# Optimization experiments

Measured on AMD Instinct MI355X. Metric: run time of the kernel, lower is better.

## Reference

```python
import jax, jax.numpy as jnp
import numpy as np

E, H, NGRAM, TM, B, NB = 1024, 16, 2, 512, 4, 32


def setup_inputs() -> dict:
    key = jax.random.key(0)
    ks = jax.random.split(key, 12)
    T3 = (NGRAM + 1) * TM
    s = 0.02
    d = {}
    d["hidden_states"] = jax.random.normal(ks[0], (T3, B, E), jnp.float32)
    d["self_attn_mask"] = jax.random.normal(ks[1], (TM, TM), jnp.float32)
    d["ngram_mask_matrix"] = jax.random.normal(ks[2], (NGRAM, 1, TM, 2 * TM), jnp.float32)
    d["i_buckets_main_stream"] = jax.random.randint(ks[3], (B, TM, TM), 0, NB, jnp.int32)
    d["i_bucket_relative_stream"] = jax.random.randint(ks[4], (B, TM, 2 * TM), 0, NB, jnp.int32)
    d["Wq"] = jax.random.normal(ks[5], (E, E), jnp.float32) * s
    d["bq"] = jnp.zeros((E,), jnp.float32)
    d["Wk"] = jax.random.normal(ks[6], (E, E), jnp.float32) * s
    d["bk"] = jnp.zeros((E,), jnp.float32)
    d["Wv"] = jax.random.normal(ks[7], (E, E), jnp.float32) * s
    d["bv"] = jnp.zeros((E,), jnp.float32)
    d["Wo"] = jax.random.normal(ks[8], (E, E), jnp.float32) * s
    d["bo"] = jnp.zeros((E,), jnp.float32)
    d["Wr"] = jax.random.normal(ks[9], (NB * H, E), jnp.float32) * s
    d["br"] = jnp.zeros((NB * H,), jnp.float32)
    return d


def _lin(x, W, b):
    return x @ W.T + b


def reference(hidden_states, self_attn_mask, ngram_mask_matrix,
              i_buckets_main_stream, i_bucket_relative_stream,
              Wq, bq, Wk, bk, Wv, bv, Wo, bo, Wr, br):
    T3, Bb, Ee = hidden_states.shape
    hd = Ee // H
    Tm = T3 // (NGRAM + 1)
    BH = Bb * H

    # projections; q is pre-scaled as in the torch module
    q = _lin(hidden_states, Wq, bq) * (hd ** -0.5)
    k = _lin(hidden_states, Wk, bk)
    v = _lin(hidden_states, Wv, bv)
    # (T3, B, E) -> (BH, T3, hd)
    q = q.reshape(T3, BH, hd).transpose(1, 0, 2)
    k = k.reshape(T3, BH, hd).transpose(1, 0, 2)
    v = v.reshape(T3, BH, hd).transpose(1, 0, 2)

    q_parts = jnp.split(q, NGRAM + 1, axis=1)
    k_parts = jnp.split(k, NGRAM + 1, axis=1)
    v_parts = jnp.split(v, NGRAM + 1, axis=1)
    h_parts = jnp.split(hidden_states, NGRAM + 1, axis=0)
    q_main, k_main, v_main, h_main = q_parts[0], k_parts[0], v_parts[0], h_parts[0]

    # ---------- main stream ----------
    aw_main = jnp.einsum('btd,bsd->bts', q_main, k_main)  # (BH, Tm, Tm)

    # relative-position logits: per-query learned bucket logits, gathered by bucket id
    vals = _lin(h_main.transpose(1, 0, 2), Wr, br)          # (B, Tm, NB*H)
    vals = vals.reshape(Bb, Tm, NB, H).transpose(0, 3, 1, 2).reshape(BH, Tm, NB)
    idx = jnp.broadcast_to(i_buckets_main_stream[:, None], (Bb, H, Tm, Tm)).reshape(BH, Tm, Tm)
    aw_main = aw_main + jnp.take_along_axis(vals, idx, axis=2) + self_attn_mask

    probs_main = jax.nn.softmax(aw_main.astype(jnp.float32), axis=-1).astype(aw_main.dtype)
    attn_main = jnp.einsum('bts,bsd->btd', probs_main, v_main)   # (BH, Tm, hd)
    attn_main = attn_main.transpose(1, 0, 2).reshape(Tm, Bb, Ee)
    attn_main = _lin(attn_main, Wo, bo)                           # (Tm, B, E)

    # ---------- ngram streams ----------
    q_ng = jnp.stack(q_parts[1:], 0)                              # (N, BH, Tm, hd)
    k_ng = jnp.stack([jnp.concatenate([k_main, kp], axis=1) for kp in k_parts[1:]], 0)  # (N, BH, 2Tm, hd)
    v_ng = jnp.stack([jnp.concatenate([v_main, vp], axis=1) for vp in v_parts[1:]], 0)
    h_ng = jnp.stack(h_parts[1:], 0)                              # (N, Tm, B, E)

    aw_ng = jnp.einsum('nbtc,nbsc->nbts', q_ng, k_ng)             # (N, BH, Tm, 2Tm)

    vals_ng = _lin(h_ng.transpose(0, 2, 1, 3), Wr, br)            # (N, B, Tm, NB*H)
    vals_ng = vals_ng.reshape(NGRAM, Bb, Tm, NB, H).transpose(0, 1, 4, 2, 3).reshape(NGRAM, BH, Tm, NB)
    idx_ng = jnp.broadcast_to(i_bucket_relative_stream[None, :, None],
                              (NGRAM, Bb, H, Tm, 2 * Tm)).reshape(NGRAM, BH, Tm, 2 * Tm)
    aw_ng = aw_ng + jnp.take_along_axis(vals_ng, idx_ng, axis=-1) + ngram_mask_matrix

    probs_ng = jax.nn.softmax(aw_ng.astype(jnp.float32), axis=-1).astype(aw_ng.dtype)
    attn_ng = jnp.einsum('nbts,nbsc->nbtc', probs_ng, v_ng)       # (N, BH, Tm, hd)
    attn_ng = attn_ng.transpose(0, 2, 1, 3).reshape(NGRAM, Tm, Bb, Ee)
    attn_ng = _lin(attn_ng, Wo, bo)                                # (N, Tm, B, E)

    attn = jnp.concatenate([attn_main[None], attn_ng], axis=0).reshape(T3, Bb, Ee)
    return attn
```

## Files before the change

kernel.cpp:

```cpp
#include <hip/hip_runtime.h>
#include <hip/hip_fp16.h>
#include <cstdint>

#define T3   1536
#define TMQ  512
#define BB   4
#define EE   1024
#define HH   16
#define HD   64
#define NBK  32
#define BHH  64

#define LOG2E 1.44269504f
#define SM_SHIFT 4.0f

typedef _Float16 half8 __attribute__((ext_vector_type(8)));
typedef float    f32x4 __attribute__((ext_vector_type(4)));

#define SWZ(r, o) ((o) ^ (((r) & 7) << 4))

__device__ inline void gl_lds16(const void* g, void* l) {
    __builtin_amdgcn_global_load_lds(
        (const __attribute__((address_space(1))) uint32_t*)g,
        (__attribute__((address_space(3))) uint32_t*)l, 16, 0, 0);
}

__global__ __launch_bounds__(256) void cvt_all(
    const float* __restrict__ hs, const float* __restrict__ Wq,
    const float* __restrict__ Wk, const float* __restrict__ Wv,
    const float* __restrict__ Wo, const float* __restrict__ Wr,
    __half* __restrict__ dst)
{
    const long i = (long)blockIdx.x * 256 + threadIdx.x;
    const float* src; long off;
    if (i < 1572864L) { src = hs; off = i; }
    else {
        const long j = i - 1572864L;
        const int  w = (int)(j >> 18);
        const long r = j & 262143L;
        src = (w == 0) ? Wq : (w == 1) ? Wk : (w == 2) ? Wv : (w == 3) ? Wo : Wr;
        off = r;
    }
    const float4 v = ((const float4*)src)[off];
    const __half2 h0 = __floats2half2_rn(v.x, v.y);
    const __half2 h1 = __floats2half2_rn(v.z, v.w);
    uint2 u;
    u.x = *(const unsigned int*)&h0;
    u.y = *(const unsigned int*)&h1;
    ((uint2*)dst)[i] = u;
}

template<int MODE>
__global__ __launch_bounds__(256) void gemm16(
    const __half* __restrict__ A,
    const __half* __restrict__ Wa, const __half* __restrict__ Wb,
    const __half* __restrict__ Wc, const __half* __restrict__ Wd,
    const float* __restrict__ ba, const float* __restrict__ bb,
    const float* __restrict__ bc, const float* __restrict__ bd,
    void* __restrict__ oa, void* __restrict__ ob,
    void* __restrict__ oc, void* __restrict__ od)
{
    __shared__ __half As[128 * 32];
    __shared__ __half Bs[128 * 32];

    const int tid  = threadIdx.x;
    const int w    = tid >> 6, lane = tid & 63;
    const int m0   = blockIdx.y * 128;

    const __half* Wsel; const float* bsel; void* osel;
    float scale, offs; int n0; int sel = 0;
    if (MODE == 0) {
        const int bx = blockIdx.x;
        sel  = (bx < 24) ? (bx >> 3) : 3;
        n0   = (bx < 24) ? (bx & 7) * 128 : (bx - 24) * 128;
        Wsel = sel == 0 ? Wa : (sel == 1 ? Wb : (sel == 2 ? Wc : Wd));
        bsel = sel == 0 ? ba : (sel == 1 ? bb : (sel == 2 ? bc : bd));
        osel = sel == 0 ? oa : (sel == 1 ? ob : (sel == 2 ? oc : od));
        scale = (sel == 0) ? 0.125f * LOG2E : (sel == 3 ? LOG2E : 1.0f);
        offs  = (sel == 3) ? -SM_SHIFT * LOG2E : 0.0f;
    } else {
        n0 = blockIdx.x * 128; Wsel = Wa; bsel = ba; osel = oa;
        scale = 1.0f; offs = 0.0f;
    }

    f32x4 acc[4][4];
    #pragma unroll
    for (int i = 0; i < 4; ++i)
        #pragma unroll
        for (int j = 0; j < 4; ++j) acc[i][j] = (f32x4){0.f, 0.f, 0.f, 0.f};

    const int wr = w >> 1, wc = w & 1;
    const int lrow = lane & 15, lkg = lane >> 4;
    const int a_off0 = (wr * 64 + lrow) * 64 + lkg * 16;
    const int b_off0 = (wc * 64 + lrow) * 64 + lkg * 16;

    const int chunkbase = w * 2048;
    const char* Ab  = (const char*)A;
    const char* Wb8 = (const char*)Wsel;

    for (int k0 = 0; k0 < EE; k0 += 32) {
        #pragma unroll
        for (int i = 0; i < 2; ++i) {
            const int off  = chunkbase + i * 1024 + lane * 16;
            const int row  = off >> 6;
            const int colb = off & 63;
            gl_lds16(Ab  + (size_t)(m0 + row) * 2048 + k0 * 2 + colb,
                     (char*)As + chunkbase + i * 1024);
            gl_lds16(Wb8 + (size_t)(n0 + row) * 2048 + k0 * 2 + colb,
                     (char*)Bs + chunkbase + i * 1024);
        }
        __syncthreads();

        half8 af[4], bf[4];
        #pragma unroll
        for (int m = 0; m < 4; ++m) af[m] = *(const half8*)((const char*)As + a_off0 + m * 1024);
        #pragma unroll
        for (int n = 0; n < 4; ++n) bf[n] = *(const half8*)((const char*)Bs + b_off0 + n * 1024);
        #pragma unroll
        for (int m = 0; m < 4; ++m)
            #pragma unroll
            for (int n = 0; n < 4; ++n)
                acc[m][n] = __builtin_amdgcn_mfma_f32_16x16x32_f16(af[m], bf[n], acc[m][n], 0, 0, 0);
        __syncthreads();
    }

    const int col_l  = lane & 15;
    const int row_l4 = (lane >> 4) * 4;
    #pragma unroll
    for (int n = 0; n < 4; ++n) {
        const int gcol = n0 + wc * 64 + n * 16 + col_l;
        const float bias = bsel[gcol];
        #pragma unroll
        for (int m = 0; m < 4; ++m) {
            #pragma unroll
            for (int j = 0; j < 4; ++j) {
                const int grow = m0 + wr * 64 + m * 16 + row_l4 + j;
                const float cval = (acc[m][n][j] + bias) * scale + offs;
                if (MODE == 0) {
                    const int t3 = grow >> 2, bb2 = grow & 3;
                    if (sel == 3) {
                        const int st = t3 >> 9, tm = t3 & 511;
                        const int nb = gcol >> 4, hh2 = gcol & 15;
                        ((float*)osel)[(((size_t)(st * BHH + bb2 * HH + hh2)) * TMQ + tm) * NBK + nb] = cval;
                    } else {
                        const int hh2 = gcol >> 6, d = gcol & 63;
                        __half* oh = (__half*)osel;
                        const __half hv = __float2half(cval);
                        if (sel == 2)
                            oh[((size_t)((bb2 * HH + hh2) * HD + d)) * T3 + t3] = hv;
                        else
                            oh[(((size_t)(bb2 * HH + hh2)) * T3 + t3) * HD + d] = hv;
                    }
                } else {
                    ((float*)osel)[(size_t)grow * EE + gcol] = cval;
                }
            }
        }
    }
}

__global__ __launch_bounds__(256) void attn_mfma(
    const __half* __restrict__ q, const __half* __restrict__ k,
    const __half* __restrict__ vt, const float* __restrict__ vals,
    const float* __restrict__ self_mask, const float* __restrict__ ngram_mask,
    const int* __restrict__ ibm, const int* __restrict__ ibr,
    __half* __restrict__ attn_pre)
{
    __shared__ __half QP [64 * 64];
    __shared__ __half Ks [64 * 64];
    __shared__ __half Vts[64 * 64];
    __shared__ float  vals_s[64 * NBK];

    const int bid = blockIdx.x;
    const int xcd = bid & 7, rr = bid >> 3;
    int s, bh, qt;
    if (rr < 128) { const int g = xcd * 128 + rr; s = 1 + (g >> 9); bh = (g >> 3) & 63; qt = g & 7; }
    else          { const int mi = xcd * 64 + (rr - 128); s = 0; bh = mi >> 3; qt = mi & 7; }
    const int b = bh >> 4, h = bh & 15;
    const int tid = threadIdx.x;
    const int w = tid >> 6, lane = tid & 63;
    const int lc = lane & 15, lg = lane >> 4;
    const int nch = (s == 0) ? 8 : 16;

    {
        const char* qg = (const char*)(q + ((size_t)bh * T3 + s * TMQ + qt * 64) * HD);
        const char* vg = (const char*)(vals + (((size_t)s * BHH + bh) * TMQ + qt * 64) * NBK);
        #pragma unroll
        for (int p = 0; p < 2; ++p) {
            const int u = tid + p * 256;
            const int row = u >> 3, sub = (u & 7) * 16;
            *(uint4*)((char*)QP + row * 128 + SWZ(row, sub)) = *(const uint4*)(qg + (size_t)u * 16);
            *(uint4*)((char*)vals_s + (size_t)u * 16)        = *(const uint4*)(vg + (size_t)u * 16);
        }
    }

    uint4 ku0, ku1, vu0, vu1;
    int   ix[4][4];
    float mk[4][4];
    {
        const char* kg = (const char*)(k + (size_t)bh * T3 * HD);
        const char* vg = (const char*)(vt + (size_t)bh * HD * T3);
        ku0 = *(const uint4*)(kg + (size_t)tid * 16);
        ku1 = *(const uint4*)(kg + (size_t)(tid + 256) * 16);
        vu0 = *(const uint4*)(vg + (size_t)(tid >> 3) * (T3 * 2) + (tid & 7) * 16);
        vu1 = *(const uint4*)(vg + (size_t)((tid + 256) >> 3) * (T3 * 2) + (tid & 7) * 16);
        #pragma unroll
        for (int j = 0; j < 4; ++j) {
            const int t = qt * 64 + w * 16 + lg * 4 + j;
            const int* ip; const float* mp;
            if (s == 0) { ip = ibm + ((size_t)b * TMQ + t) * TMQ + lc;
                          mp = self_mask + (size_t)t * TMQ + lc; }
            else        { ip = ibr + ((size_t)b * TMQ + t) * (2 * TMQ) + lc;
                          mp = ngram_mask + ((size_t)(s - 1) * TMQ + t) * (2 * TMQ) + lc; }
            #pragma unroll
            for (int n = 0; n < 4; ++n) { ix[j][n] = ip[n * 16]; mk[j][n] = mp[n * 16]; }
        }
    }
    __syncthreads();

    half8 aq[2];
    {
        const int qr = w * 16 + lc;
        const char* qb = (const char*)QP + qr * 128;
        aq[0] = *(const half8*)(qb + SWZ(qr, lg * 16));
        aq[1] = *(const half8*)(qb + SWZ(qr, 64 + lg * 16));
    }

    f32x4 o[4];
    #pragma unroll
    for (int nd = 0; nd < 4; ++nd) o[nd] = (f32x4){0.f, 0.f, 0.f, 0.f};
    float l_p[4] = {0.f, 0.f, 0.f, 0.f};

    for (int c = 0; c < nch; ++c) {
        if (c > 0) __syncthreads();
        {
            const int u0 = tid, u1 = tid + 256;
            const int r0 = u0 >> 3, s0 = (u0 & 7) * 16;
            const int r1 = u1 >> 3, s1 = (u1 & 7) * 16;
            *(uint4*)((char*)Ks  + r0 * 128 + SWZ(r0, s0)) = ku0;
            *(uint4*)((char*)Ks  + r1 * 128 + SWZ(r1, s1)) = ku1;
            *(uint4*)((char*)Vts + r0 * 128 + SWZ(r0, s0)) = vu0;
            *(uint4*)((char*)Vts + r1 * 128 + SWZ(r1, s1)) = vu1;
        }
        __syncthreads();

        if (c + 1 < nch) {
            const int jn  = (c + 1) * 64;
            const int t3n = (jn < TMQ) ? jn : s * TMQ + (jn - TMQ);
            const char* kg = (const char*)(k + ((size_t)bh * T3 + t3n) * HD);
            const char* vg = (const char*)(vt + (size_t)bh * HD * T3 + t3n);
            ku0 = *(const uint4*)(kg + (size_t)tid * 16);
            ku1 = *(const uint4*)(kg + (size_t)(tid + 256) * 16);
            vu0 = *(const uint4*)(vg + (size_t)(tid >> 3) * (T3 * 2) + (tid & 7) * 16);
            vu1 = *(const uint4*)(vg + (size_t)((tid + 256) >> 3) * (T3 * 2) + (tid & 7) * 16);
        }

        f32x4 sc[4];
        #pragma unroll
        for (int n = 0; n < 4; ++n) sc[n] = (f32x4){0.f, 0.f, 0.f, 0.f};
        __builtin_amdgcn_s_setprio(1);
        #pragma unroll
        for (int ks = 0; ks < 2; ++ks) {
            #pragma unroll
            for (int n = 0; n < 4; ++n) {
                const int kr = n * 16 + lc;
                const half8 bk = *(const half8*)((const char*)Ks + kr * 128 + SWZ(kr, ks * 64 + lg * 16));
                sc[n] = __builtin_amdgcn_mfma_f32_16x16x32_f16(aq[ks], bk, sc[n], 0, 0, 0);
            }
        }
        __builtin_amdgcn_s_setprio(0);

        #pragma unroll
        for (int j = 0; j < 4; ++j) {
            const int ql = w * 16 + lg * 4 + j;
            const float* vr = vals_s + ql * NBK;
            float p[4];
            #pragma unroll
            for (int n = 0; n < 4; ++n) {
                const float sv = fmaf(mk[j][n], LOG2E, sc[n][j] + vr[ix[j][n]]);
                p[n] = __builtin_amdgcn_exp2f(sv);
            }
            l_p[j] += (p[0] + p[1]) + (p[2] + p[3]);
            char* pb = (char*)QP + ql * 128;
            *(__half*)(pb + SWZ(ql, (0 * 16 + lc) * 2)) = __float2half(p[0]);
            *(__half*)(pb + SWZ(ql, (1 * 16 + lc) * 2)) = __float2half(p[1]);
            *(__half*)(pb + SWZ(ql, (2 * 16 + lc) * 2)) = __float2half(p[2]);
            *(__half*)(pb + SWZ(ql, (3 * 16 + lc) * 2)) = __float2half(p[3]);
        }

        if (c + 1 < nch) {
            const int jn = (c + 1) * 64;
            #pragma unroll
            for (int j = 0; j < 4; ++j) {
                const int t = qt * 64 + w * 16 + lg * 4 + j;
                const int* ip; const float* mp;
                if (s == 0) { ip = ibm + ((size_t)b * TMQ + t) * TMQ + jn + lc;
                              mp = self_mask + (size_t)t * TMQ + jn + lc; }
                else        { ip = ibr + ((size_t)b * TMQ + t) * (2 * TMQ) + jn + lc;
                              mp = ngram_mask + ((size_t)(s - 1) * TMQ + t) * (2 * TMQ) + jn + lc; }
                #pragma unroll
                for (int n = 0; n < 4; ++n) { ix[j][n] = ip[n * 16]; mk[j][n] = mp[n * 16]; }
            }
        }
        __threadfence_block();

        __builtin_amdgcn_s_setprio(1);
        #pragma unroll
        for (int ks = 0; ks < 2; ++ks) {
            const int ar = w * 16 + lc;
            const half8 ap = *(const half8*)((const char*)QP + ar * 128 + SWZ(ar, ks * 64 + lg * 16));
            #pragma unroll
            for (int nd = 0; nd < 4; ++nd) {
                const int vr2 = nd * 16 + lc;
                const half8 bv = *(const half8*)((const char*)Vts + vr2 * 128 + SWZ(vr2, ks * 64 + lg * 16));
                o[nd] = __builtin_amdgcn_mfma_f32_16x16x32_f16(ap, bv, o[nd], 0, 0, 0);
            }
        }
        __builtin_amdgcn_s_setprio(0);
    }

    #pragma unroll
    for (int j = 0; j < 4; ++j) {
        float l = l_p[j];
        l += __shfl_xor(l, 1);
        l += __shfl_xor(l, 2);
        l += __shfl_xor(l, 4);
        l += __shfl_xor(l, 8);
        const float inv = 1.0f / l;
        const int t = qt * 64 + w * 16 + lg * 4 + j;
        __half* op = attn_pre + (((size_t)(s * TMQ + t)) * BB + b) * EE + h * HD + lc;
        #pragma unroll
        for (int nd = 0; nd < 4; ++nd)
            op[nd * 16] = __float2half(o[nd][j] * inv);
    }
}

extern "C" void kernel_launch(void* const* d_in, const int* in_sizes, int n_in,
                              void* d_out, int out_size, void* d_ws, size_t ws_size,
                              hipStream_t stream)
{
    const float* hs    = (const float*)d_in[0];
    const float* smask = (const float*)d_in[1];
    const float* nmask = (const float*)d_in[2];
    const int*   ibm   = (const int*)d_in[3];
    const int*   ibr   = (const int*)d_in[4];
    const float* Wq = (const float*)d_in[5];
    const float* bq = (const float*)d_in[6];
    const float* Wk = (const float*)d_in[7];
    const float* bk = (const float*)d_in[8];
    const float* Wv = (const float*)d_in[9];
    const float* bv = (const float*)d_in[10];
    const float* Wo = (const float*)d_in[11];
    const float* bo = (const float*)d_in[12];
    const float* Wr = (const float*)d_in[13];
    const float* br = (const float*)d_in[14];
    float* out = (float*)d_out;

    const size_t NQKV = (size_t)BHH * T3 * HD;
    __half* qh    = (__half*)d_ws;
    __half* kh    = qh + NQKV;
    __half* vth   = kh + NQKV;
    float*  valsw = (float*)(vth + NQKV);
    __half* hs_h  = (__half*)(valsw + (size_t)3 * BHH * TMQ * NBK);
    __half* apre_h = hs_h;
    __half* Wq_h = hs_h + (size_t)T3 * BB * EE;
    __half* Wk_h = Wq_h + (size_t)EE * EE;
    __half* Wv_h = Wk_h + (size_t)EE * EE;
    __half* Wo_h = Wv_h + (size_t)EE * EE;
    __half* Wr_h = Wo_h + (size_t)EE * EE;

    dim3 blk(256);
    cvt_all<<<dim3(10752), blk, 0, stream>>>(hs, Wq, Wk, Wv, Wo, Wr, hs_h);

    gemm16<0><<<dim3(28, 48), blk, 0, stream>>>(hs_h, Wq_h, Wk_h, Wv_h, Wr_h,
                                                bq, bk, bv, br,
                                                qh, kh, vth, valsw);
    attn_mfma<<<dim3(1536), blk, 0, stream>>>(qh, kh, vth, valsw, smask, nmask,
                                              ibm, ibr, apre_h);
    gemm16<2><<<dim3(8, 48), blk, 0, stream>>>(apre_h, Wo_h, nullptr, nullptr, nullptr,
                                               bo, nullptr, nullptr, nullptr,
                                               out, nullptr, nullptr, nullptr);
}
```

Baseline: 210.1 us.

## Double GEMM K-tile to 64 and add XOR-swizzled LDS layout

The fp16 projection GEMM now stages 64-wide K slices of A and W into LDS per iteration instead of 32, which halves the number of loop iterations and barrier pairs. The global-to-LDS copy permutes 16-byte column chunks by row (an XOR swizzle), and the fragment reads undo that permutation to avoid LDS bank conflicts. LDS use doubles to 32 KB per block, which may limit how many blocks fit on each CU.

```diff
diff --git a/kernel.cpp b/kernel.cpp
--- a/kernel.cpp
+++ b/kernel.cpp
@@ -60,8 +60,8 @@
     void* __restrict__ oa, void* __restrict__ ob,
     void* __restrict__ oc, void* __restrict__ od)
 {
-    __shared__ __half As[128 * 32];
-    __shared__ __half Bs[128 * 32];
+    __shared__ __half As[128 * 64];
+    __shared__ __half Bs[128 * 64];
 
     const int tid  = threadIdx.x;
     const int w    = tid >> 6, lane = tid & 63;
@@ -91,36 +91,47 @@
 
     const int wr = w >> 1, wc = w & 1;
     const int lrow = lane & 15, lkg = lane >> 4;
-    const int a_off0 = (wr * 64 + lrow) * 64 + lkg * 16;
-    const int b_off0 = (wc * 64 + lrow) * 64 + lkg * 16;
-
-    const int chunkbase = w * 2048;
+    const int aoff = (wr * 64 + lrow) * 128;
+    const int boff = (wc * 64 + lrow) * 128;
+    const int rswz = (lrow & 7) << 4;
+
+    const int tilebase = w * 4096;
     const char* Ab  = (const char*)A;
     const char* Wb8 = (const char*)Wsel;
-
-    for (int k0 = 0; k0 < EE; k0 += 32) {
-        #pragma unroll
-        for (int i = 0; i < 2; ++i) {
-            const int off  = chunkbase + i * 1024 + lane * 16;
-            const int row  = off >> 6;
-            const int colb = off & 63;
-            gl_lds16(Ab  + (size_t)(m0 + row) * 2048 + k0 * 2 + colb,
-                     (char*)As + chunkbase + i * 1024);
-            gl_lds16(Wb8 + (size_t)(n0 + row) * 2048 + k0 * 2 + colb,
-                     (char*)Bs + chunkbase + i * 1024);
+    int srow[4], scol[4];
+    #pragma unroll
+    for (int i = 0; i < 4; ++i) {
+        const int off = tilebase + i * 1024 + lane * 16;
+        srow[i] = off >> 7;
+        scol[i] = (((off >> 4) & 7) ^ (srow[i] & 7)) * 16;
+    }
+
+    for (int k0 = 0; k0 < EE; k0 += 64) {
+        #pragma unroll
+        for (int i = 0; i < 4; ++i) {
+            gl_lds16(Ab  + (size_t)(m0 + srow[i]) * 2048 + k0 * 2 + scol[i],
+                     (char*)As + tilebase + i * 1024);
+            gl_lds16(Wb8 + (size_t)(n0 + srow[i]) * 2048 + k0 * 2 + scol[i],
+                     (char*)Bs + tilebase + i * 1024);
         }
         __syncthreads();
 
-        half8 af[4], bf[4];
-        #pragma unroll
-        for (int m = 0; m < 4; ++m) af[m] = *(const half8*)((const char*)As + a_off0 + m * 1024);
-        #pragma unroll
-        for (int n = 0; n < 4; ++n) bf[n] = *(const half8*)((const char*)Bs + b_off0 + n * 1024);
-        #pragma unroll
-        for (int m = 0; m < 4; ++m)
+        #pragma unroll
+        for (int ks = 0; ks < 2; ++ks) {
+            const int kb = (ks * 64 + lkg * 16) ^ rswz;
+            half8 af[4], bf[4];
+            #pragma unroll
+            for (int m = 0; m < 4; ++m)
+                af[m] = *(const half8*)((const char*)As + aoff + m * 2048 + kb);
             #pragma unroll
             for (int n = 0; n < 4; ++n)
-                acc[m][n] = __builtin_amdgcn_mfma_f32_16x16x32_f16(af[m], bf[n], acc[m][n], 0, 0, 0);
+                bf[n] = *(const half8*)((const char*)Bs + boff + n * 2048 + kb);
+            #pragma unroll
+            for (int m = 0; m < 4; ++m)
+                #pragma unroll
+                for (int n = 0; n < 4; ++n)
+                    acc[m][n] = __builtin_amdgcn_mfma_f32_16x16x32_f16(af[m], bf[n], acc[m][n], 0, 0, 0);
+        }
         __syncthreads();
     }
 
```

Result: faster. 204.8 us (-2.5%).

## Double-buffer GEMM LDS staging and swizzle K-chunks to avoid bank conflicts

Applied to the files above, without the earlier changes.

The projection GEMM kernel now uses two LDS buffers, so global-to-LDS loads for the next K slice are issued while MFMAs consume the current slice. It also XOR-swizzles the 16-byte K chunk position by row, applied on the global source address side, to reduce LDS bank conflicts on fragment reads. This doubles the LDS footprint per block, which could lower occupancy, and relies on the barriers ordering the async global_load_lds writes correctly.

```diff
diff --git a/kernel.cpp b/kernel.cpp
--- a/kernel.cpp
+++ b/kernel.cpp
@@ -60,8 +60,8 @@
     void* __restrict__ oa, void* __restrict__ ob,
     void* __restrict__ oc, void* __restrict__ od)
 {
-    __shared__ __half As[128 * 32];
-    __shared__ __half Bs[128 * 32];
+    __shared__ __half As0[128 * 32], Bs0[128 * 32];
+    __shared__ __half As1[128 * 32], Bs1[128 * 32];
 
     const int tid  = threadIdx.x;
     const int w    = tid >> 6, lane = tid & 63;
@@ -91,38 +91,60 @@
 
     const int wr = w >> 1, wc = w & 1;
     const int lrow = lane & 15, lkg = lane >> 4;
-    const int a_off0 = (wr * 64 + lrow) * 64 + lkg * 16;
-    const int b_off0 = (wc * 64 + lrow) * 64 + lkg * 16;
-
-    const int chunkbase = w * 2048;
+    const int aoff  = (wr * 64 + lrow) * 64;
+    const int boff  = (wc * 64 + lrow) * 64;
+    const int kbase = ((lkg ^ (lrow & 3)) << 4);
+
+    const int stb0 = w * 2048, stb1 = w * 2048 + 1024;
+    const int off0 = stb0 + lane * 16, off1 = stb1 + lane * 16;
+    const int srow0 = off0 >> 6, srow1 = off1 >> 6;
+    const int scol0 = ((((off0 >> 4) & 3) ^ (srow0 & 3)) << 4);
+    const int scol1 = ((((off1 >> 4) & 3) ^ (srow1 & 3)) << 4);
     const char* Ab  = (const char*)A;
     const char* Wb8 = (const char*)Wsel;
 
-    for (int k0 = 0; k0 < EE; k0 += 32) {
-        #pragma unroll
-        for (int i = 0; i < 2; ++i) {
-            const int off  = chunkbase + i * 1024 + lane * 16;
-            const int row  = off >> 6;
-            const int colb = off & 63;
-            gl_lds16(Ab  + (size_t)(m0 + row) * 2048 + k0 * 2 + colb,
-                     (char*)As + chunkbase + i * 1024);
-            gl_lds16(Wb8 + (size_t)(n0 + row) * 2048 + k0 * 2 + colb,
-                     (char*)Bs + chunkbase + i * 1024);
-        }
+#define STAGEK(AS, BS, K0) do {                                                   \
+    gl_lds16(Ab  + (size_t)(m0 + srow0) * 2048 + (size_t)(K0) * 2 + scol0,        \
+             (char*)(AS) + stb0);                                                 \
+    gl_lds16(Wb8 + (size_t)(n0 + srow0) * 2048 + (size_t)(K0) * 2 + scol0,        \
+             (char*)(BS) + stb0);                                                 \
+    gl_lds16(Ab  + (size_t)(m0 + srow1) * 2048 + (size_t)(K0) * 2 + scol1,        \
+             (char*)(AS) + stb1);                                                 \
+    gl_lds16(Wb8 + (size_t)(n0 + srow1) * 2048 + (size_t)(K0) * 2 + scol1,        \
+             (char*)(BS) + stb1);                                                 \
+} while (0)
+
+#define COMPUTEK(AS, BS) do {                                                     \
+    half8 af[4], bf[4];                                                           \
+    _Pragma("unroll")                                                             \
+    for (int m = 0; m < 4; ++m)                                                   \
+        af[m] = *(const half8*)((const char*)(AS) + aoff + m * 1024 + kbase);     \
+    _Pragma("unroll")                                                             \
+    for (int n = 0; n < 4; ++n)                                                   \
+        bf[n] = *(const half8*)((const char*)(BS) + boff + n * 1024 + kbase);     \
+    _Pragma("unroll")                                                             \
+    for (int m = 0; m < 4; ++m)                                                   \
+        _Pragma("unroll")                                                         \
+        for (int n = 0; n < 4; ++n)                                               \
+            acc[m][n] = __builtin_amdgcn_mfma_f32_16x16x32_f16(af[m], bf[n],      \
+                                                               acc[m][n], 0, 0, 0);\
+} while (0)
+
+    STAGEK(As0, Bs0, 0);
+    __syncthreads();
+
+    for (int t = 0; t < 16; ++t) {
+        const int k0 = t * 64;
+        STAGEK(As1, Bs1, k0 + 32);
+        COMPUTEK(As0, Bs0);
         __syncthreads();
-
-        half8 af[4], bf[4];
-        #pragma unroll
-        for (int m = 0; m < 4; ++m) af[m] = *(const half8*)((const char*)As + a_off0 + m * 1024);
-        #pragma unroll
-        for (int n = 0; n < 4; ++n) bf[n] = *(const half8*)((const char*)Bs + b_off0 + n * 1024);
-        #pragma unroll
-        for (int m = 0; m < 4; ++m)
-            #pragma unroll
-            for (int n = 0; n < 4; ++n)
-                acc[m][n] = __builtin_amdgcn_mfma_f32_16x16x32_f16(af[m], bf[n], acc[m][n], 0, 0, 0);
+        if (t < 15) STAGEK(As0, Bs0, k0 + 64);
+        COMPUTEK(As1, Bs1);
         __syncthreads();
     }
+
+#undef STAGEK
+#undef COMPUTEK
 
     const int col_l  = lane & 15;
     const int row_l4 = (lane >> 4) * 4;
```

Result: slower. 215.0 us (+2.3%).
